# Kernel optimization log

Hardware: AMD Instinct MI355X
Metric: run time of the kernel (lower is better)

## Reference

```python
import jax, jax.numpy as jnp
import numpy as np

D_MODEL = 1024
N_HEADS = 16
HEAD_DIM = D_MODEL // N_HEADS
WINDOW = 256
NEG_INF = -1e30  # finite stand-in for -inf; identical softmax result, NaN-safe


def setup_inputs() -> dict:
    key = jax.random.key(0)
    ks = jax.random.split(key, 5)
    B, L = 1, 4096
    s = 1.0 / np.sqrt(D_MODEL)
    return {
        "x": jax.random.normal(ks[0], (B, L, D_MODEL), dtype=jnp.float32),
        "Wq": jax.random.normal(ks[1], (D_MODEL, D_MODEL), dtype=jnp.float32) * s,
        "Wk": jax.random.normal(ks[2], (D_MODEL, D_MODEL), dtype=jnp.float32) * s,
        "Wv": jax.random.normal(ks[3], (D_MODEL, D_MODEL), dtype=jnp.float32) * s,
        "Wo": jax.random.normal(ks[4], (D_MODEL, D_MODEL), dtype=jnp.float32) * s,
    }


def reference(x, Wq, Wk, Wv, Wo):
    B, L, _ = x.shape
    # projections (nn.Linear applies x @ W.T; weights here are stored as [out,in])
    q = (x @ Wq.T).reshape(B, L, N_HEADS, HEAD_DIM).transpose(0, 2, 1, 3)  # [B,H,L,Dh]
    k = (x @ Wk.T).reshape(B, L, N_HEADS, HEAD_DIM).transpose(0, 2, 1, 3)
    v = (x @ Wv.T).reshape(B, L, N_HEADS, HEAD_DIM).transpose(0, 2, 1, 3)

    # sliding-window causal mask: position i attends to j in [i-WINDOW+1, i]
    i = jnp.arange(L)[:, None]
    j = jnp.arange(L)[None, :]
    allowed = (j <= i) & (j >= i - WINDOW + 1)  # [L,L] bool

    scale = 1.0 / jnp.sqrt(jnp.asarray(HEAD_DIM, dtype=q.dtype))
    scores = jnp.einsum("bhqd,bhkd->bhqk", q, k) * scale  # [B,H,L,L]
    scores = jnp.where(allowed, scores, NEG_INF)
    attn = jax.nn.softmax(scores, axis=-1)
    out = jnp.einsum("bhqk,bhkd->bhqd", attn, v)  # [B,H,L,Dh]
    out = out.transpose(0, 2, 1, 3).reshape(B, L, D_MODEL)
    return out @ Wo.T
```

## Files before the change

kernel.cpp:

```cpp
#include <hip/hip_runtime.h>

using bf16x8 = __attribute__((ext_vector_type(8))) short;
using u16x8  = __attribute__((ext_vector_type(8))) unsigned short;
using f32x4  = __attribute__((ext_vector_type(4))) float;

#define LSEQ   4096
#define NH     16
#define DH     64
#define WIN    256
#define DM     1024

__device__ __forceinline__ void gl2lds16(const void* g, void* l) {
  __builtin_amdgcn_global_load_lds(
      (const __attribute__((address_space(1))) unsigned int*)g,
      (__attribute__((address_space(3))) unsigned int*)l,
      16, 0, 0);
}

__device__ __forceinline__ unsigned short f2bf(float f) {
  unsigned int u = __float_as_uint(f);
  u += 0x7fffu + ((u >> 16) & 1u);
  return (unsigned short)(u >> 16);
}

__global__ __launch_bounds__(256) void cvt_all(
    const float* __restrict__ x,  const float* __restrict__ wq,
    const float* __restrict__ wk, const float* __restrict__ wv,
    const float* __restrict__ wo, unsigned short* __restrict__ dst)
{
  const size_t i = ((size_t)blockIdx.x * 256 + threadIdx.x) * 8;
  const size_t XN = (size_t)LSEQ * DM;
  const float* src;
  size_t off;
  if (i < XN) { src = x; off = i; }
  else {
    const size_t j = i - XN;
    const int s = (int)(j >> 20);
    off = j & ((1u << 20) - 1);
    src = (s == 0) ? wq : (s == 1) ? wk : (s == 2) ? wv : wo;
  }
  const f32x4 f0 = *(const f32x4*)(src + off);
  const f32x4 f1 = *(const f32x4*)(src + off + 4);
  u16x8 o;
  o[0] = f2bf(f0[0]); o[1] = f2bf(f0[1]); o[2] = f2bf(f0[2]); o[3] = f2bf(f0[3]);
  o[4] = f2bf(f1[0]); o[5] = f2bf(f1[1]); o[6] = f2bf(f1[2]); o[7] = f2bf(f1[3]);
  *(u16x8*)(dst + i) = o;
}

__device__ __forceinline__ void gemm_tile(
    const unsigned short* __restrict__ X,
    const unsigned short* __restrict__ W,
    int m0, int n0,
    unsigned short* As, unsigned short* Bs,
    f32x4 (&acc)[4][4])
{
  const int tid  = threadIdx.x;
  const int lane = tid & 63;
  const int wave = tid >> 6;
  const int wm = wave >> 1, wn = wave & 1;
  const int fr = lane & 15, quad = lane >> 4;

  const f32x4 zero = {0.f, 0.f, 0.f, 0.f};
  #pragma unroll
  for (int i = 0; i < 4; ++i)
    #pragma unroll
    for (int j = 0; j < 4; ++j)
      acc[i][j] = zero;

  const int c0 = tid, c1 = tid + 256;
  const unsigned short* xa0 = X + (size_t)(m0 + (c0 >> 2)) * DM + (c0 & 3) * 8;
  const unsigned short* xa1 = X + (size_t)(m0 + (c1 >> 2)) * DM + (c1 & 3) * 8;
  const unsigned short* wb0 = W + (size_t)(n0 + (c0 >> 2)) * DM + (c0 & 3) * 8;
  const unsigned short* wb1 = W + (size_t)(n0 + (c1 >> 2)) * DM + (c1 & 3) * 8;
  char* la0 = (char*)As + c0 * 16;
  char* la1 = (char*)As + c1 * 16;
  char* lb0 = (char*)Bs + c0 * 16;
  char* lb1 = (char*)Bs + c1 * 16;

  for (int kt = 0; kt < DM; kt += 32) {
    gl2lds16(xa0 + kt, la0);
    gl2lds16(xa1 + kt, la1);
    gl2lds16(wb0 + kt, lb0);
    gl2lds16(wb1 + kt, lb1);
    __syncthreads();

    bf16x8 a[4], b[4];
    #pragma unroll
    for (int t = 0; t < 4; ++t)
      a[t] = *(const bf16x8*)(As + (wm * 64 + t * 16 + fr) * 32 + quad * 8);
    #pragma unroll
    for (int t = 0; t < 4; ++t)
      b[t] = *(const bf16x8*)(Bs + (wn * 64 + t * 16 + fr) * 32 + quad * 8);

    #pragma unroll
    for (int i = 0; i < 4; ++i)
      #pragma unroll
      for (int j = 0; j < 4; ++j)
        acc[i][j] = __builtin_amdgcn_mfma_f32_16x16x32_bf16(a[i], b[j], acc[i][j], 0, 0, 0);
    __syncthreads();
  }
}

__global__ __launch_bounds__(256) void proj_gemm(
    const unsigned short* __restrict__ X,
    const unsigned short* __restrict__ Wq,
    const unsigned short* __restrict__ Wk,
    const unsigned short* __restrict__ Wv,
    unsigned short* __restrict__ Qo,
    unsigned short* __restrict__ Ko,
    unsigned short* __restrict__ Vt)
{
  __shared__ unsigned short As[128 * 32];
  __shared__ unsigned short Bs[128 * 32];
  const int id = blockIdx.x;
  const int lane = threadIdx.x & 63;
  const int wave = threadIdx.x >> 6;
  const int wm = wave >> 1, wn = wave & 1;
  const int cn = lane & 15, quad = lane >> 4;
  f32x4 acc[4][4];

  if (id < 512) {
    const int m0   = (id & 31) * 128;
    const int by   = id >> 5;
    const int wsel = by >> 3;
    const int n0   = (by & 7) * 128;
    gemm_tile(X, wsel ? Wk : Wq, m0, n0, As, Bs, acc);

    const float qscl = wsel ? 1.0f : 0.180336881f;
    unsigned short* O = wsel ? Ko : Qo;
    #pragma unroll
    for (int i = 0; i < 4; ++i)
      #pragma unroll
      for (int j = 0; j < 4; ++j)
        #pragma unroll
        for (int r = 0; r < 4; ++r) {
          const int row = m0 + wm * 64 + i * 16 + quad * 4 + r;
          const int col = n0 + wn * 64 + j * 16 + cn;
          const int h = col >> 6, d = col & 63;
          O[(size_t)(h * LSEQ + row) * DH + d] = f2bf(acc[i][j][r] * qscl);
        }
  } else {
    const int vid = id - 512;
    const int m0 = (vid & 7) * 128;
    const int n0 = (vid >> 3) * 128;
    gemm_tile(Wv, X, m0, n0, As, Bs, acc);

    #pragma unroll
    for (int i = 0; i < 4; ++i)
      #pragma unroll
      for (int j = 0; j < 4; ++j)
        #pragma unroll
        for (int r = 0; r < 4; ++r) {
          const int row = m0 + wm * 64 + i * 16 + quad * 4 + r;
          const int col = n0 + wn * 64 + j * 16 + cn;
          Vt[(size_t)row * LSEQ + col] = f2bf(acc[i][j][r]);
        }
  }
}

__global__ __launch_bounds__(256) void out_gemm(
    const unsigned short* __restrict__ X,
    const unsigned short* __restrict__ W,
    float* __restrict__ O)
{
  __shared__ unsigned short As2[64 * 32];
  __shared__ unsigned short Bs[128 * 32];
  const int m0 = blockIdx.x * 64;
  const int n0 = blockIdx.y * 128;
  const int tid  = threadIdx.x;
  const int lane = tid & 63;
  const int wave = tid >> 6;
  const int wm = wave >> 1, wn = wave & 1;
  const int fr = lane & 15, quad = lane >> 4;

  const f32x4 zero = {0.f, 0.f, 0.f, 0.f};
  f32x4 acc[2][4];
  #pragma unroll
  for (int i = 0; i < 2; ++i)
    #pragma unroll
    for (int j = 0; j < 4; ++j)
      acc[i][j] = zero;

  const unsigned short* xa  = X + (size_t)(m0 + (tid >> 2)) * DM + (tid & 3) * 8;
  const unsigned short* wb0 = W + (size_t)(n0 + (tid >> 2)) * DM + (tid & 3) * 8;
  const unsigned short* wb1 = W + (size_t)(n0 + ((tid + 256) >> 2)) * DM + (tid & 3) * 8;
  char* la  = (char*)As2 + tid * 16;
  char* lb0 = (char*)Bs + tid * 16;
  char* lb1 = (char*)Bs + (tid + 256) * 16;

  for (int kt = 0; kt < DM; kt += 32) {
    gl2lds16(xa + kt, la);
    gl2lds16(wb0 + kt, lb0);
    gl2lds16(wb1 + kt, lb1);
    __syncthreads();

    bf16x8 a[2], b[4];
    #pragma unroll
    for (int t = 0; t < 2; ++t)
      a[t] = *(const bf16x8*)(As2 + (wm * 32 + t * 16 + fr) * 32 + quad * 8);
    #pragma unroll
    for (int t = 0; t < 4; ++t)
      b[t] = *(const bf16x8*)(Bs + (wn * 64 + t * 16 + fr) * 32 + quad * 8);

    #pragma unroll
    for (int i = 0; i < 2; ++i)
      #pragma unroll
      for (int j = 0; j < 4; ++j)
        acc[i][j] = __builtin_amdgcn_mfma_f32_16x16x32_bf16(a[i], b[j], acc[i][j], 0, 0, 0);
    __syncthreads();
  }

  const int cn = lane & 15;
  #pragma unroll
  for (int i = 0; i < 2; ++i)
    #pragma unroll
    for (int j = 0; j < 4; ++j)
      #pragma unroll
      for (int r = 0; r < 4; ++r) {
        const int row = m0 + wm * 32 + i * 16 + quad * 4 + r;
        const int col = n0 + wn * 64 + j * 16 + cn;
        O[(size_t)row * DM + col] = acc[i][j][r];
      }
}

#define PSTR 80
__global__ __launch_bounds__(256) void attn_fwd(
    const unsigned short* __restrict__ Q,
    const unsigned short* __restrict__ K,
    const unsigned short* __restrict__ Vt,
    unsigned short* __restrict__ Oa)
{
  __shared__ unsigned short Pl[4][16 * PSTR];
  const int h    = blockIdx.y;
  const int bq0  = blockIdx.x * 64;
  const int wave = threadIdx.x >> 6;
  const int lane = threadIdx.x & 63;
  const int n = lane & 15, quad = lane >> 4;
  const int q0 = bq0 + wave * 16;
  unsigned short* pl = Pl[wave];

  const size_t qbase = ((size_t)(h * LSEQ + q0 + n)) * DH + quad * 8;
  const bf16x8 aq0 = *(const bf16x8*)(Q + qbase);
  const bf16x8 aq1 = *(const bf16x8*)(Q + qbase + 32);

  const f32x4 zero = {0.f, 0.f, 0.f, 0.f};
  f32x4 acc[4] = {zero, zero, zero, zero};
  float li[4] = {0.f, 0.f, 0.f, 0.f};

  const int jb0 = (bq0 >= WIN) ? (bq0 - WIN) : 0;
  for (int jb = jb0; jb < bq0 + 64; jb += 64) {
    f32x4 s[4];
    #pragma unroll
    for (int u = 0; u < 4; ++u) {
      const int j0 = jb + u * 16;
      const size_t kbase = ((size_t)(h * LSEQ + j0 + n)) * DH + quad * 8;
      const bf16x8 kb0 = *(const bf16x8*)(K + kbase);
      const bf16x8 kb1 = *(const bf16x8*)(K + kbase + 32);
      f32x4 c = zero;
      c = __builtin_amdgcn_mfma_f32_16x16x32_bf16(aq0, kb0, c, 0, 0, 0);
      c = __builtin_amdgcn_mfma_f32_16x16x32_bf16(aq1, kb1, c, 0, 0, 0);
      s[u] = c;
    }
    #pragma unroll
    for (int u = 0; u < 4; ++u)
      #pragma unroll
      for (int r = 0; r < 4; ++r) {
        const int qi = q0 + quad * 4 + r;
        const int kj = jb + u * 16 + n;
        const bool ok = (kj <= qi) && (kj + WIN > qi);
        const float e = __builtin_exp2f(ok ? s[u][r] - 32.0f : -1e30f);
        s[u][r] = e;
        li[r] += e;
      }
    #pragma unroll
    for (int u = 0; u < 4; ++u)
      #pragma unroll
      for (int r = 0; r < 4; ++r)
        pl[(quad * 4 + r) * PSTR + u * 16 + n] = f2bf(s[u][r]);
    asm volatile("s_waitcnt lgkmcnt(0)" ::: "memory");
    const bf16x8 pa0 = *(const bf16x8*)(pl + n * PSTR + quad * 8);
    const bf16x8 pa1 = *(const bf16x8*)(pl + n * PSTR + 32 + quad * 8);
    #pragma unroll
    for (int ct = 0; ct < 4; ++ct) {
      const size_t vb = ((size_t)(h * DH + ct * 16 + n)) * LSEQ + jb + quad * 8;
      const bf16x8 vb0 = *(const bf16x8*)(Vt + vb);
      const bf16x8 vb1 = *(const bf16x8*)(Vt + vb + 32);
      acc[ct] = __builtin_amdgcn_mfma_f32_16x16x32_bf16(pa0, vb0, acc[ct], 0, 0, 0);
      acc[ct] = __builtin_amdgcn_mfma_f32_16x16x32_bf16(pa1, vb1, acc[ct], 0, 0, 0);
    }
  }

  float rd[4];
  #pragma unroll
  for (int r = 0; r < 4; ++r) {
    float v = li[r];
    v += __shfl_xor(v, 1);
    v += __shfl_xor(v, 2);
    v += __shfl_xor(v, 4);
    v += __shfl_xor(v, 8);
    rd[r] = 1.0f / v;
  }
  #pragma unroll
  for (int ct = 0; ct < 4; ++ct)
    #pragma unroll
    for (int r = 0; r < 4; ++r) {
      const int row = q0 + quad * 4 + r;
      const int col = h * DH + ct * 16 + n;
      Oa[(size_t)row * DM + col] = f2bf(acc[ct][r] * rd[r]);
    }
}

extern "C" void kernel_launch(void* const* d_in, const int* in_sizes, int n_in,
                              void* d_out, int out_size, void* d_ws, size_t ws_size,
                              hipStream_t stream) {
  const float* x  = (const float*)d_in[0];
  const float* Wq = (const float*)d_in[1];
  const float* Wk = (const float*)d_in[2];
  const float* Wv = (const float*)d_in[3];
  const float* Wo = (const float*)d_in[4];
  float* out = (float*)d_out;

  unsigned short* xb  = (unsigned short*)d_ws;
  unsigned short* Wqb = xb  + (size_t)LSEQ * DM;
  unsigned short* Wkb = Wqb + (size_t)DM * DM;
  unsigned short* Wvb = Wkb + (size_t)DM * DM;
  unsigned short* Wob = Wvb + (size_t)DM * DM;
  unsigned short* Q    = Wob + (size_t)DM * DM;
  unsigned short* K    = Q   + (size_t)LSEQ * DM;
  unsigned short* Vt   = K   + (size_t)LSEQ * DM;
  unsigned short* Attn = Vt  + (size_t)LSEQ * DM;

  cvt_all<<<dim3(4096), 256, 0, stream>>>(x, Wq, Wk, Wv, Wo, xb);
  proj_gemm<<<dim3(768), 256, 0, stream>>>(xb, Wqb, Wkb, Wvb, Q, K, Vt);
  attn_fwd<<<dim3(64, 16), 256, 0, stream>>>(Q, K, Vt, Attn);
  out_gemm<<<dim3(64, 8), 256, 0, stream>>>(Attn, Wob, out);
}
```

Baseline: 175.7 us.

## Split attention key range across two waves per 16-query tile with LDS combine

Each block now handles one 16-row query tile with two waves. The waves split that tile's key tiles, restricted to the ones inside the sliding window, and the partial accumulators and row sums are merged through shared memory. Before, each wave scanned every key tile of its 64-query block. The change is meant to cut wasted masked key tiles and add parallelism, giving 4096 small blocks. Block ids are remapped so 8 heads sit next to each other, which may help K/V cache reuse. The cost is a shared-memory reduction, a barrier, and less reuse of K and V across queries within a block.

```diff
diff --git a/kernel.cpp b/kernel.cpp
--- a/kernel.cpp
+++ b/kernel.cpp
@@ -223,37 +223,45 @@
       }
 }
 
-#define PSTR 80
-__global__ __launch_bounds__(256) void attn_fwd(
+#define PSTR 72
+__global__ __launch_bounds__(128) void attn_fwd(
     const unsigned short* __restrict__ Q,
     const unsigned short* __restrict__ K,
     const unsigned short* __restrict__ Vt,
     unsigned short* __restrict__ Oa)
 {
-  __shared__ unsigned short Pl[4][16 * PSTR];
-  const int h    = blockIdx.y;
-  const int bq0  = blockIdx.x * 64;
+  __shared__ unsigned short Pl[2][16 * PSTR];
+  __shared__ float Cmb[16][65];
+  __shared__ float Lmb[16];
+  const int id   = blockIdx.x;
+  const int h    = (id & 7) | ((id >> 11) << 3);
+  const int qt   = (id >> 3) & 255;
+  const int q0   = qt * 16;
   const int wave = threadIdx.x >> 6;
   const int lane = threadIdx.x & 63;
   const int n = lane & 15, quad = lane >> 4;
-  const int q0 = bq0 + wave * 16;
   unsigned short* pl = Pl[wave];
 
   const size_t qbase = ((size_t)(h * LSEQ + q0 + n)) * DH + quad * 8;
   const bf16x8 aq0 = *(const bf16x8*)(Q + qbase);
   const bf16x8 aq1 = *(const bf16x8*)(Q + qbase + 32);
 
+  const int lo = (q0 >= 255) ? ((q0 - 255) & ~63) : 0;
+  const int hi = (q0 + 15) & ~63;
+  const int ntile = ((hi - lo) >> 6) + 1;
+  const int nw0 = (ntile + 1) >> 1;
+  const int tb = (wave == 0) ? lo : lo + nw0 * 64;
+  const int te = (wave == 0) ? lo + nw0 * 64 : hi + 64;
+
   const f32x4 zero = {0.f, 0.f, 0.f, 0.f};
   f32x4 acc[4] = {zero, zero, zero, zero};
   float li[4] = {0.f, 0.f, 0.f, 0.f};
 
-  const int jb0 = (bq0 >= WIN) ? (bq0 - WIN) : 0;
-  for (int jb = jb0; jb < bq0 + 64; jb += 64) {
+  for (int jb = tb; jb < te; jb += 64) {
     f32x4 s[4];
     #pragma unroll
     for (int u = 0; u < 4; ++u) {
-      const int j0 = jb + u * 16;
-      const size_t kbase = ((size_t)(h * LSEQ + j0 + n)) * DH + quad * 8;
+      const size_t kbase = ((size_t)(h * LSEQ + jb + u * 16 + n)) * DH + quad * 8;
       const bf16x8 kb0 = *(const bf16x8*)(K + kbase);
       const bf16x8 kb1 = *(const bf16x8*)(K + kbase + 32);
       f32x4 c = zero;
@@ -290,7 +298,7 @@
     }
   }
 
-  float rd[4];
+  float lr[4];
   #pragma unroll
   for (int r = 0; r < 4; ++r) {
     float v = li[r];
@@ -298,16 +306,37 @@
     v += __shfl_xor(v, 2);
     v += __shfl_xor(v, 4);
     v += __shfl_xor(v, 8);
-    rd[r] = 1.0f / v;
-  }
-  #pragma unroll
-  for (int ct = 0; ct < 4; ++ct)
-    #pragma unroll
-    for (int r = 0; r < 4; ++r) {
-      const int row = q0 + quad * 4 + r;
-      const int col = h * DH + ct * 16 + n;
-      Oa[(size_t)row * DM + col] = f2bf(acc[ct][r] * rd[r]);
+    lr[r] = v;
+  }
+
+  if (wave == 1) {
+    #pragma unroll
+    for (int ct = 0; ct < 4; ++ct)
+      #pragma unroll
+      for (int r = 0; r < 4; ++r)
+        Cmb[quad * 4 + r][ct * 16 + n] = acc[ct][r];
+    if (n == 0) {
+      #pragma unroll
+      for (int r = 0; r < 4; ++r)
+        Lmb[quad * 4 + r] = lr[r];
     }
+  }
+  __syncthreads();
+  if (wave == 0) {
+    float rd[4];
+    #pragma unroll
+    for (int r = 0; r < 4; ++r)
+      rd[r] = 1.0f / (lr[r] + Lmb[quad * 4 + r]);
+    #pragma unroll
+    for (int ct = 0; ct < 4; ++ct)
+      #pragma unroll
+      for (int r = 0; r < 4; ++r) {
+        const int row = q0 + quad * 4 + r;
+        const int col = h * DH + ct * 16 + n;
+        const float o = (acc[ct][r] + Cmb[quad * 4 + r][ct * 16 + n]) * rd[r];
+        Oa[(size_t)row * DM + col] = f2bf(o);
+      }
+  }
 }
 
 extern "C" void kernel_launch(void* const* d_in, const int* in_sizes, int n_in,
@@ -332,6 +361,6 @@
 
   cvt_all<<<dim3(4096), 256, 0, stream>>>(x, Wq, Wk, Wv, Wo, xb);
   proj_gemm<<<dim3(768), 256, 0, stream>>>(xb, Wqb, Wkb, Wvb, Q, K, Vt);
-  attn_fwd<<<dim3(64, 16), 256, 0, stream>>>(Q, K, Vt, Attn);
+  attn_fwd<<<dim3(4096), 128, 0, stream>>>(Q, K, Vt, Attn);
   out_gemm<<<dim3(64, 8), 256, 0, stream>>>(Attn, Wob, out);
 }
```

Result: no change. 174.0 us (-0.9%).

## Stage K/V tiles in double-buffered LDS shared across waves in attention

Applied to the files above, without the earlier changes.

In the attention kernel, the four waves of a block now share one K tile and one V tile staged in LDS, instead of each wave loading them directly from global memory. The buffers are double-buffered, with the next tile prefetched into registers while the current one is used. The grid becomes 1-D with a remapped block index so neighbouring blocks take different heads, and the LDS row stride shrinks to 72. This cuts redundant global and L2 traffic for K/V, at the cost of extra LDS use and a block-wide barrier on every iteration.

```diff
diff --git a/kernel.cpp b/kernel.cpp
--- a/kernel.cpp
+++ b/kernel.cpp
@@ -223,18 +223,22 @@
       }
 }
 
-#define PSTR 80
+#define PSTR 72
 __global__ __launch_bounds__(256) void attn_fwd(
     const unsigned short* __restrict__ Q,
     const unsigned short* __restrict__ K,
     const unsigned short* __restrict__ Vt,
     unsigned short* __restrict__ Oa)
 {
+  __shared__ unsigned short Ks[2][64 * PSTR];
+  __shared__ unsigned short Vs[2][64 * PSTR];
   __shared__ unsigned short Pl[4][16 * PSTR];
-  const int h    = blockIdx.y;
-  const int bq0  = blockIdx.x * 64;
-  const int wave = threadIdx.x >> 6;
-  const int lane = threadIdx.x & 63;
+  const int id   = blockIdx.x;
+  const int h    = (id & 7) | ((id >> 9) << 3);
+  const int bq0  = ((id >> 3) & 63) * 64;
+  const int tid  = threadIdx.x;
+  const int wave = tid >> 6;
+  const int lane = tid & 63;
   const int n = lane & 15, quad = lane >> 4;
   const int q0 = bq0 + wave * 16;
   unsigned short* pl = Pl[wave];
@@ -243,19 +247,51 @@
   const bf16x8 aq0 = *(const bf16x8*)(Q + qbase);
   const bf16x8 aq1 = *(const bf16x8*)(Q + qbase + 32);
 
+  const int lo = (bq0 >= WIN) ? (bq0 - WIN) : 0;
+
+  const int c0 = tid, c1 = tid + 256;
+  const size_t kg0 = ((size_t)(h * LSEQ + (c0 >> 3))) * DH + (c0 & 7) * 8;
+  const size_t kg1 = ((size_t)(h * LSEQ + (c1 >> 3))) * DH + (c1 & 7) * 8;
+  const size_t vg0 = ((size_t)(h * DH + (c0 >> 3))) * LSEQ + (c0 & 7) * 8;
+  const size_t vg1 = ((size_t)(h * DH + (c1 >> 3))) * LSEQ + (c1 & 7) * 8;
+  const int ld0 = (c0 >> 3) * PSTR + (c0 & 7) * 8;
+  const int ld1 = (c1 >> 3) * PSTR + (c1 & 7) * 8;
+
+  {
+    const bf16x8 ka = *(const bf16x8*)(K  + kg0 + (size_t)lo * DH);
+    const bf16x8 kc = *(const bf16x8*)(K  + kg1 + (size_t)lo * DH);
+    const bf16x8 va = *(const bf16x8*)(Vt + vg0 + lo);
+    const bf16x8 vc = *(const bf16x8*)(Vt + vg1 + lo);
+    *(bf16x8*)(Ks[0] + ld0) = ka;
+    *(bf16x8*)(Ks[0] + ld1) = kc;
+    *(bf16x8*)(Vs[0] + ld0) = va;
+    *(bf16x8*)(Vs[0] + ld1) = vc;
+  }
+  __syncthreads();
+
   const f32x4 zero = {0.f, 0.f, 0.f, 0.f};
   f32x4 acc[4] = {zero, zero, zero, zero};
   float li[4] = {0.f, 0.f, 0.f, 0.f};
 
-  const int jb0 = (bq0 >= WIN) ? (bq0 - WIN) : 0;
-  for (int jb = jb0; jb < bq0 + 64; jb += 64) {
+  int t = 0;
+  for (int jb = lo; jb < bq0 + 64; jb += 64, ++t) {
+    const int buf = t & 1;
+    const bool more = (jb + 64 < bq0 + 64);
+    bf16x8 nk0, nk1, nv0, nv1;
+    if (more) {
+      const int jn = jb + 64;
+      nk0 = *(const bf16x8*)(K  + kg0 + (size_t)jn * DH);
+      nk1 = *(const bf16x8*)(K  + kg1 + (size_t)jn * DH);
+      nv0 = *(const bf16x8*)(Vt + vg0 + jn);
+      nv1 = *(const bf16x8*)(Vt + vg1 + jn);
+    }
+    const unsigned short* ks = Ks[buf];
+    const unsigned short* vs = Vs[buf];
     f32x4 s[4];
     #pragma unroll
     for (int u = 0; u < 4; ++u) {
-      const int j0 = jb + u * 16;
-      const size_t kbase = ((size_t)(h * LSEQ + j0 + n)) * DH + quad * 8;
-      const bf16x8 kb0 = *(const bf16x8*)(K + kbase);
-      const bf16x8 kb1 = *(const bf16x8*)(K + kbase + 32);
+      const bf16x8 kb0 = *(const bf16x8*)(ks + (u * 16 + n) * PSTR + quad * 8);
+      const bf16x8 kb1 = *(const bf16x8*)(ks + (u * 16 + n) * PSTR + 32 + quad * 8);
       f32x4 c = zero;
       c = __builtin_amdgcn_mfma_f32_16x16x32_bf16(aq0, kb0, c, 0, 0, 0);
       c = __builtin_amdgcn_mfma_f32_16x16x32_bf16(aq1, kb1, c, 0, 0, 0);
@@ -282,12 +318,18 @@
     const bf16x8 pa1 = *(const bf16x8*)(pl + n * PSTR + 32 + quad * 8);
     #pragma unroll
     for (int ct = 0; ct < 4; ++ct) {
-      const size_t vb = ((size_t)(h * DH + ct * 16 + n)) * LSEQ + jb + quad * 8;
-      const bf16x8 vb0 = *(const bf16x8*)(Vt + vb);
-      const bf16x8 vb1 = *(const bf16x8*)(Vt + vb + 32);
+      const bf16x8 vb0 = *(const bf16x8*)(vs + (ct * 16 + n) * PSTR + quad * 8);
+      const bf16x8 vb1 = *(const bf16x8*)(vs + (ct * 16 + n) * PSTR + 32 + quad * 8);
       acc[ct] = __builtin_amdgcn_mfma_f32_16x16x32_bf16(pa0, vb0, acc[ct], 0, 0, 0);
       acc[ct] = __builtin_amdgcn_mfma_f32_16x16x32_bf16(pa1, vb1, acc[ct], 0, 0, 0);
     }
+    if (more) {
+      *(bf16x8*)(Ks[buf ^ 1] + ld0) = nk0;
+      *(bf16x8*)(Ks[buf ^ 1] + ld1) = nk1;
+      *(bf16x8*)(Vs[buf ^ 1] + ld0) = nv0;
+      *(bf16x8*)(Vs[buf ^ 1] + ld1) = nv1;
+    }
+    __syncthreads();
   }
 
   float rd[4];
@@ -332,6 +374,6 @@
 
   cvt_all<<<dim3(4096), 256, 0, stream>>>(x, Wq, Wk, Wv, Wo, xb);
   proj_gemm<<<dim3(768), 256, 0, stream>>>(xb, Wqb, Wkb, Wvb, Q, K, Vt);
-  attn_fwd<<<dim3(64, 16), 256, 0, stream>>>(Q, K, Vt, Attn);
+  attn_fwd<<<dim3(1024), 256, 0, stream>>>(Q, K, Vt, Attn);
   out_gemm<<<dim3(64, 8), 256, 0, stream>>>(Attn, Wob, out);
 }
```

Result: faster. 156.4 us (-11.0%).
